# Optimization experiments

Measured on AMD Instinct MI355X. Metric: run time of the kernel, lower is better.

## Reference

```python
import jax, jax.numpy as jnp
import numpy as np
from jax import lax

B, N, D_FEAT = 16, 4096, 20
NPOINT, NSAMPLE = 1024, 32
MLP = [64, 64, 128]
IN_CH = 3 + 1 + D_FEAT  # grouped_xyz_norm(3) + L2 norm(1) + grouped_depth_norm(20)
BN_EPS = 1e-5


def setup_inputs() -> dict:
    key = jax.random.key(0)
    ks = jax.random.split(key, 20)
    inp = {
        "xyz": jax.random.normal(ks[0], (B, 3, N), dtype=jnp.float32),
        "feature": jax.random.normal(ks[1], (B, N, D_FEAT), dtype=jnp.float32),
    }
    last = IN_CH
    kidx = 2
    for li, out_ch in enumerate(MLP):
        inp[f"w{li}"] = jax.random.normal(ks[kidx], (out_ch, last), dtype=jnp.float32) * (1.0 / np.sqrt(last)); kidx += 1
        inp[f"b{li}"] = jax.random.normal(ks[kidx], (out_ch,), dtype=jnp.float32) * 0.01; kidx += 1
        inp[f"g{li}"] = 1.0 + 0.1 * jax.random.normal(ks[kidx], (out_ch,), dtype=jnp.float32); kidx += 1
        inp[f"bt{li}"] = 0.1 * jax.random.normal(ks[kidx], (out_ch,), dtype=jnp.float32); kidx += 1
        last = out_ch
    return inp


def square_distance(src, dst):
    # [B,S,C] x [B,M,C] -> [B,S,M]
    d = -2.0 * jnp.einsum("bsc,bmc->bsm", src, dst)
    d = d + jnp.sum(src * src, -1)[:, :, None]
    d = d + jnp.sum(dst * dst, -1)[:, None, :]
    return d


def farthest_point_sample(pts, npoint):
    # pts: [B,N,C]; deterministic start at index 0 (torch uses random start)
    b, n, _ = pts.shape
    bidx = jnp.arange(b)

    def step(carry, _):
        dist, far = carry
        centroid = pts[bidx, far]                      # [B,C]
        d = jnp.sum((pts - centroid[:, None, :]) ** 2, -1)  # [B,N]
        dist = jnp.minimum(dist, d)
        nxt = jnp.argmax(dist, -1)
        return (dist, nxt), far

    init = (jnp.full((b, n), 1e10, pts.dtype), jnp.zeros((b,), jnp.int32))
    _, idx = lax.scan(step, init, None, length=npoint)
    return idx.T  # [B,npoint]


def _gather_groups(points, idx):
    # points [B,N,C], idx [B,S,K] -> [B,S,K,C]
    return jax.vmap(lambda p, i: p[i])(points, idx)


def conv_bn_relu(x, w, b, g, bt):
    # x [B,C,K,S]; 1x1 conv = channel matmul; BN in training mode (batch stats, biased var)
    y = jnp.einsum("bcks,oc->boks", x, w) + b[None, :, None, None]
    mu = jnp.mean(y, axis=(0, 2, 3), keepdims=True)
    var = jnp.mean((y - mu) ** 2, axis=(0, 2, 3), keepdims=True)
    y = (y - mu) * lax.rsqrt(var + BN_EPS)
    y = y * g[None, :, None, None] + bt[None, :, None, None]
    return jax.nn.relu(y)


def reference(xyz, feature, w0, b0, g0, bt0, w1, b1, g1, bt1, w2, b2, g2, bt2):
    xyz_n = jnp.transpose(xyz, (0, 2, 1))              # [B,N,3]
    combined = jnp.concatenate([xyz_n, feature], -1)   # [B,N,23]
    fps_idx = farthest_point_sample(combined, NPOINT)  # [B,S]

    new_bin = jnp.take_along_axis(feature, fps_idx[:, :, None], axis=1)  # [B,S,20]
    new_xyz = jnp.take_along_axis(xyz_n, fps_idx[:, :, None], axis=1)    # [B,S,3]

    sqd = square_distance(new_bin, feature) + square_distance(new_xyz, xyz_n)  # [B,S,N]
    idx = jnp.argsort(sqd, axis=-1)[:, :, :NSAMPLE]    # [B,S,K]

    gxyz = _gather_groups(xyz_n, idx)                  # [B,S,K,3]
    gfeat = _gather_groups(feature, idx)               # [B,S,K,20]
    gxyz_norm = gxyz - new_xyz[:, :, None, :]
    gdep_norm = gfeat - new_bin[:, :, None, :]
    nrm = jnp.sqrt(jnp.maximum(jnp.sum(gxyz_norm ** 2, -1, keepdims=True), 1e-12))
    new_points = jnp.concatenate([gxyz_norm, nrm, gdep_norm], -1)  # [B,S,K,24]

    x = jnp.transpose(new_points, (0, 3, 2, 1))        # [B,24,K,S]
    for (w, b, g, bt) in [(w0, b0, g0, bt0), (w1, b1, g1, bt1), (w2, b2, g2, bt2)]:
        x = conv_bn_relu(x, w, b, g, bt)
    out = jnp.max(x, axis=2)                           # [B,128,S]
    return jnp.transpose(new_xyz, (0, 2, 1)), out, new_bin
```

## Files before the change

kernel.cpp:

```cpp
#include <hip/hip_runtime.h>

#define BB 16
#define NN 4096
#define DFEAT 20
#define SS 1024
#define KK 32
#define MM (BB*SS*KK)

#define WS_STATS   0ull
#define WS_PARAMS  8192ull
#define WS_FPSIDX  12288ull
#define WS_CENT    81920ull
#define WS_KNN     1654784ull
#define WS_COMB    3751936ull
#define WS_YB      10043392ull
#define WS_NEED    77152256ull

typedef float v2f __attribute__((ext_vector_type(2)));

static __device__ __forceinline__ unsigned short f2bf(float f){
    unsigned u = __float_as_uint(f);
    unsigned r = (u + 0x7FFFu + ((u >> 16) & 1u)) >> 16;
    return (unsigned short)r;
}
static __device__ __forceinline__ float bf2f(unsigned short v){
    return __uint_as_float((unsigned)v << 16);
}
static __device__ __forceinline__ void pinv2(v2f& x){
    asm volatile("" : "+v"(x));
}

template<int CTRL>
static __device__ __forceinline__ unsigned dpp32_or0(unsigned x){
    return (unsigned)__builtin_amdgcn_update_dpp(0, (int)x, CTRL, 0xf, 0xf, true);
}
static __device__ __forceinline__ unsigned umax32(unsigned a, unsigned b){
    return a > b ? a : b;
}
static __device__ __forceinline__ unsigned wave_max_u32(unsigned x){
    x = umax32(x, dpp32_or0<0x111>(x));
    x = umax32(x, dpp32_or0<0x112>(x));
    x = umax32(x, dpp32_or0<0x114>(x));
    x = umax32(x, dpp32_or0<0x118>(x));
    x = umax32(x, dpp32_or0<0x142>(x));
    x = umax32(x, dpp32_or0<0x143>(x));
    return x;
}

__global__ void k_zstats(double* __restrict__ stats){
    int t = threadIdx.x;
#pragma unroll
    for (int i = 0; i < 4; ++i) stats[i*256 + t] = 0.0;
}

__global__ void k_fail(float* __restrict__ out, int n){
    int i = blockIdx.x * 256 + threadIdx.x;
    if (i < n) out[i] = 0.f;
}

__global__ __launch_bounds__(256) void k_build(const float* __restrict__ xyz,
                                               const float* __restrict__ feat,
                                               float* __restrict__ comb)
{
    int idx = blockIdx.x * 256 + threadIdx.x;
    int b = idx >> 12, j = idx & 4095;
    float c[24];
    c[0] = xyz[((size_t)b*3 + 0)*NN + j];
    c[1] = xyz[((size_t)b*3 + 1)*NN + j];
    c[2] = xyz[((size_t)b*3 + 2)*NN + j];
    const float* f = feat + ((size_t)b*NN + j)*DFEAT;
#pragma unroll
    for (int d = 0; d < 20; ++d) c[3+d] = f[d];
    c[23] = 0.f;
    float* out = comb + (size_t)idx * 24;
#pragma unroll
    for (int q = 0; q < 6; ++q)
        ((float4*)out)[q] = make_float4(c[4*q], c[4*q+1], c[4*q+2], c[4*q+3]);
}

__global__ __launch_bounds__(512, 2) void k_fps(const float* __restrict__ comb,
                                                int* __restrict__ fpsidx)
{
    int b = blockIdx.x, t = threadIdx.x;
    const float* C = comb + (size_t)b * NN * 24;
    v2f pt2[4][24];
    v2f dist2[4];
#pragma unroll
    for (int p = 0; p < 8; ++p){
        const float4* r = (const float4*)(C + (size_t)(t + 512*p) * 24);
#pragma unroll
        for (int q = 0; q < 6; ++q){
            float4 v = r[q];
            pt2[p>>1][4*q+0][p&1] = v.x;
            pt2[p>>1][4*q+1][p&1] = v.y;
            pt2[p>>1][4*q+2][p&1] = v.z;
            pt2[p>>1][4*q+3][p&1] = v.w;
        }
    }
#pragma unroll
    for (int k = 0; k < 4; ++k){
        dist2[k] = (v2f){1e10f, 1e10f};
#pragma unroll
        for (int q = 0; q < 23; ++q) pinv2(pt2[k][q]);
    }

    __shared__ __align__(16) float wpt[2][8][24];
    __shared__ unsigned long long gkey[4];
    __shared__ int fps_lds[SS];
    int lane = t & 63, w = t >> 6;
    unsigned nt = 0xFFFFFFFFu - (unsigned)t;
    int far = 0;

    if (t < 4) gkey[t] = 0ull;

    float cc[24];
    {
        const float4* crow = (const float4*)C;
#pragma unroll
        for (int q = 0; q < 6; ++q){
            float4 cv = crow[q];
            cc[4*q] = cv.x; cc[4*q+1] = cv.y; cc[4*q+2] = cv.z; cc[4*q+3] = cv.w;
        }
    }
    __syncthreads();

    for (int s = 0; s < SS; ++s){
        if (t == 0) fps_lds[s] = far;
        v2f acc2[4];
#pragma unroll
        for (int k = 0; k < 4; ++k){
            v2f d0 = pt2[k][0] - cc[0];
            acc2[k] = d0 * d0;
        }
#pragma unroll
        for (int q = 1; q < 23; ++q){
            float cq = cc[q];
#pragma unroll
            for (int k = 0; k < 4; ++k){
                v2f dd = pt2[k][q] - cq;
                acc2[k] = __builtin_elementwise_fma(dd, dd, acc2[k]);
            }
        }
#pragma unroll
        for (int k = 0; k < 4; ++k)
            dist2[k] = __builtin_elementwise_min(dist2[k], acc2[k]);
        v2f m01 = __builtin_elementwise_max(dist2[0], dist2[1]);
        v2f m23 = __builtin_elementwise_max(dist2[2], dist2[3]);
        v2f mt  = __builtin_elementwise_max(m01, m23);
        float mf = fmaxf(mt[0], mt[1]);
        unsigned maxbits = __float_as_uint(mf);
        int pstar = 0;
#pragma unroll
        for (int p = 7; p >= 0; --p)
            if (__float_as_uint(dist2[p>>1][p&1]) == maxbits) pstar = p;

        unsigned M = __builtin_amdgcn_readlane((int)wave_max_u32(maxbits), 63);
        unsigned cidx = (maxbits == M) ? (nt - ((unsigned)pstar << 9)) : 0u;
        unsigned widxc = __builtin_amdgcn_readlane((int)wave_max_u32(cidx), 63);
        unsigned widx  = 0xFFFFFFFFu - widxc;

        int par = s & 1;
        if (t == (int)(widx & 511u)){
            int pw = (int)(widx >> 9);
            float* dst = wpt[par][w];
            switch (pw){
#define PE(P,q) pt2[(P)>>1][q][(P)&1]
#define STASH(P) case P: \
                ((float4*)dst)[0] = make_float4(PE(P,0),PE(P,1),PE(P,2),PE(P,3)); \
                ((float4*)dst)[1] = make_float4(PE(P,4),PE(P,5),PE(P,6),PE(P,7)); \
                ((float4*)dst)[2] = make_float4(PE(P,8),PE(P,9),PE(P,10),PE(P,11)); \
                ((float4*)dst)[3] = make_float4(PE(P,12),PE(P,13),PE(P,14),PE(P,15)); \
                ((float4*)dst)[4] = make_float4(PE(P,16),PE(P,17),PE(P,18),PE(P,19)); \
                ((float4*)dst)[5] = make_float4(PE(P,20),PE(P,21),PE(P,22),0.f); \
                break;
            STASH(0) STASH(1) STASH(2) STASH(3)
            STASH(4) STASH(5) STASH(6) STASH(7)
#undef STASH
#undef PE
            }
        }
        if (lane == 63){
            unsigned long long key = ((unsigned long long)M << 32)
                                   | (unsigned long long)widxc;
            atomicMax(&gkey[s & 3], key);
        }
        __syncthreads();
        unsigned long long k2 = gkey[s & 3];
        if (t == 0) gkey[(s + 2) & 3] = 0ull;
        far = (int)(0xFFFFFFFFu - (unsigned)(k2 & 0xFFFFFFFFull));
        int wg = (far & 511) >> 6;
        const float4* crow = (const float4*)wpt[par][wg];
#pragma unroll
        for (int q = 0; q < 6; ++q){
            float4 cv = crow[q];
            cc[4*q] = cv.x; cc[4*q+1] = cv.y; cc[4*q+2] = cv.z; cc[4*q+3] = cv.w;
        }
    }
    __syncthreads();
    fpsidx[b*SS + t]        = fps_lds[t];
    fpsidx[b*SS + 512 + t]  = fps_lds[512 + t];
}

__global__ __launch_bounds__(256) void k_gather(const float* __restrict__ comb,
                                                const int* __restrict__ fpsidx,
                                                float* __restrict__ cent,
                                                float* __restrict__ out0,
                                                float* __restrict__ out2)
{
    int idx = blockIdx.x * 256 + threadIdx.x;
    int b = idx >> 10, s = idx & 1023;
    int j = fpsidx[idx];
    const float* row = comb + ((size_t)b*NN + j) * 24;
    float* cr = cent + (size_t)idx * 24;
#pragma unroll
    for (int q = 0; q < 6; ++q) ((float4*)cr)[q] = ((const float4*)row)[q];
#pragma unroll
    for (int c = 0; c < 3; ++c) out0[((size_t)b*3 + c)*SS + s] = row[c];
    float* o2 = out2 + (size_t)idx * 20;
#pragma unroll
    for (int d = 0; d < 20; ++d) o2[d] = row[3 + d];
}

__global__ __launch_bounds__(256) void k_knn(const float* __restrict__ comb,
                                             const float* __restrict__ cent,
                                             int* __restrict__ knn)
{
    int w = threadIdx.x >> 6, lane = threadIdx.x & 63;
    int r = blockIdx.x * 4 + w;
    int b = r >> 10;
    const float* crow = cent + (size_t)r * 24;
    const float* P0 = comb + (size_t)b * NN * 24;
    double cc[24];
#pragma unroll
    for (int q = 0; q < 24; ++q) cc[q] = (double)crow[q];
    unsigned u[64];
#pragma unroll
    for (int k = 0; k < 64; ++k){
        int j = k*64 + lane;
        const float4* pr = (const float4*)(P0 + (size_t)j * 24);
        double acc = 0.0;
#pragma unroll
        for (int q = 0; q < 6; ++q){
            float4 v = pr[q];
            double d0 = (double)v.x - cc[4*q];
            double d1 = (double)v.y - cc[4*q+1];
            double d2 = (double)v.z - cc[4*q+2];
            double d3 = (double)v.w - cc[4*q+3];
            acc += d0*d0; acc += d1*d1; acc += d2*d2; acc += d3*d3;
        }
        u[k] = __float_as_uint((float)acc);
    }
    unsigned lo = 0u, hi = 0xFFFFFFFFu;
    for (int it = 0; it < 32; ++it){
        unsigned mid = lo + ((hi - lo) >> 1);
        int cnt = 0;
#pragma unroll
        for (int k = 0; k < 64; ++k) cnt += (u[k] <= mid) ? 1 : 0;
#pragma unroll
        for (int off = 32; off > 0; off >>= 1) cnt += __shfl_xor(cnt, off);
        if (cnt >= KK) hi = mid; else lo = mid + 1;
    }
    unsigned T = lo;
    int* orow = knn + (size_t)r * KK;
    unsigned long long lmask = (1ull << lane) - 1ull;
    int pos = 0;
#pragma unroll
    for (int k = 0; k < 64; ++k){
        bool lt = (u[k] < T);
        unsigned long long mk = __ballot(lt);
        if (lt) orow[pos + __popcll(mk & lmask)] = k*64 + lane;
        pos += __popcll(mk);
    }
#pragma unroll
    for (int k = 0; k < 64; ++k){
        if (pos >= KK) break;
        bool eq = (u[k] == T);
        unsigned long long mk = __ballot(eq);
        int rk = __popcll(mk & lmask);
        if (eq && (pos + rk) < KK) orow[pos + rk] = k*64 + lane;
        pos += __popcll(mk);
    }
}

__global__ __launch_bounds__(256) void k_l1(const float* __restrict__ comb,
                                            const float* __restrict__ cent,
                                            const int* __restrict__ knn,
                                            const float* __restrict__ w0,
                                            const float* __restrict__ b0,
                                            unsigned short* __restrict__ yb)
{
    __shared__ float Wt[24][64];
    __shared__ float Xt[24][68];
    int t = threadIdx.x;
    int m_base = blockIdx.x * 64;
    for (int i = t; i < 1536; i += 256){
        int o = i / 24, c = i - o*24;
        Wt[c][o] = w0[i];
    }
    {
        int sm = t & 63, g = t >> 6;
        int m = m_base + sm;
        int b = m >> 15;
        int row = m >> 5;
        int j = knn[m];
        const float* P  = comb + ((size_t)b*NN + j) * 24;
        const float* Cc = cent + (size_t)row * 24;
        if (g == 0){
            float dx = P[0]-Cc[0], dy = P[1]-Cc[1], dz = P[2]-Cc[2];
            Xt[0][sm] = dx; Xt[1][sm] = dy; Xt[2][sm] = dz;
            float n2 = dx*dx; n2 = fmaf(dy, dy, n2); n2 = fmaf(dz, dz, n2);
            Xt[3][sm] = sqrtf(fmaxf(n2, 1e-12f));
            Xt[4][sm] = P[3] - Cc[3];
            Xt[5][sm] = P[4] - Cc[4];
        } else {
#pragma unroll
            for (int cq = 0; cq < 6; ++cq){
                int c = 6*g + cq;
                Xt[c][sm] = P[c-1] - Cc[c-1];
            }
        }
    }
    __syncthreads();
    int i = t >> 4, jj = t & 15;
    float acc[4][4] = {};
#pragma unroll
    for (int c = 0; c < 24; ++c){
        float4 wv = *(const float4*)&Wt[c][i*4];
        float4 xv = *(const float4*)&Xt[c][jj*4];
        float wr[4] = {wv.x, wv.y, wv.z, wv.w};
        float xr[4] = {xv.x, xv.y, xv.z, xv.w};
#pragma unroll
        for (int a = 0; a < 4; ++a)
#pragma unroll
            for (int q = 0; q < 4; ++q) acc[a][q] = fmaf(wr[a], xr[q], acc[a][q]);
    }
#pragma unroll
    for (int oi = 0; oi < 4; ++oi){
        int o = i*4 + oi;
        float bb = b0[o];
        ushort4 rv;
        rv.x = f2bf(acc[oi][0]+bb); rv.y = f2bf(acc[oi][1]+bb);
        rv.z = f2bf(acc[oi][2]+bb); rv.w = f2bf(acc[oi][3]+bb);
        *(ushort4*)&yb[(size_t)o*MM + m_base + jj*4] = rv;
    }
}

__global__ __launch_bounds__(256) void k_stats(const unsigned short* __restrict__ y,
                                               double* __restrict__ stats)
{
    const int chunks = 8;
    int c = blockIdx.x / chunks, ch = blockIdx.x % chunks;
    size_t base = (size_t)c * MM + (size_t)ch * (MM / chunks);
    double s1 = 0.0, s2 = 0.0;
    const unsigned short* p = y + base;
    for (int i = threadIdx.x; i < MM/chunks; i += 256){
        float v = bf2f(p[i]);
        s1 += v; s2 += (double)v * v;
    }
#pragma unroll
    for (int off = 32; off > 0; off >>= 1){
        s1 += __shfl_xor(s1, off);
        s2 += __shfl_xor(s2, off);
    }
    __shared__ double ps1[4], ps2[4];
    int w = threadIdx.x >> 6, lane = threadIdx.x & 63;
    if (lane == 0){ ps1[w] = s1; ps2[w] = s2; }
    __syncthreads();
    if (threadIdx.x == 0){
        atomicAdd(&stats[c*2 + 0], ps1[0]+ps1[1]+ps1[2]+ps1[3]);
        atomicAdd(&stats[c*2 + 1], ps2[0]+ps2[1]+ps2[2]+ps2[3]);
    }
}

__global__ void k_affine(const double* __restrict__ stats, float* __restrict__ params, int C)
{
    int c = threadIdx.x;
    if (c < C){
        double mu = stats[c*2] / (double)MM;
        double var = stats[c*2 + 1] / (double)MM - mu*mu;
        params[c*2 + 0] = (float)mu;
        params[c*2 + 1] = (float)(1.0 / sqrt(var + 1e-5));
    }
}

__global__ __launch_bounds__(256) void k_l2(unsigned short* __restrict__ yb,
                                            const float* __restrict__ prm,
                                            const float* __restrict__ gg,
                                            const float* __restrict__ bt,
                                            const float* __restrict__ w,
                                            const float* __restrict__ bias)
{
    __shared__ float Wt[64][64];
    __shared__ float Xt[64][68];
    int t = threadIdx.x;
    int m_base = blockIdx.x * 64;
    for (int i = t; i < 4096; i += 256){
        int o = i >> 6, c = i & 63;
        Wt[c][o] = w[i];
    }
#pragma unroll
    for (int rp = 0; rp < 16; ++rp){
        int idx = rp*256 + t;
        int c = idx >> 6, mm2 = idx & 63;
        float v = bf2f(yb[(size_t)c*MM + m_base + mm2]);
        float t1 = (v - prm[c*2]) * prm[c*2 + 1];
        Xt[c][mm2] = fmaxf(fmaf(t1, gg[c], bt[c]), 0.f);
    }
    __syncthreads();
    int i = t >> 4, jj = t & 15;
    float acc[4][4] = {};
#pragma unroll
    for (int c = 0; c < 64; ++c){
        float4 wv = *(const float4*)&Wt[c][i*4];
        float4 xv = *(const float4*)&Xt[c][jj*4];
        float wr[4] = {wv.x, wv.y, wv.z, wv.w};
        float xr[4] = {xv.x, xv.y, xv.z, xv.w};
#pragma unroll
        for (int a = 0; a < 4; ++a)
#pragma unroll
            for (int q = 0; q < 4; ++q) acc[a][q] = fmaf(wr[a], xr[q], acc[a][q]);
    }
#pragma unroll
    for (int oi = 0; oi < 4; ++oi){
        int o = i*4 + oi;
        float bb = bias[o];
        ushort4 rv;
        rv.x = f2bf(acc[oi][0]+bb); rv.y = f2bf(acc[oi][1]+bb);
        rv.z = f2bf(acc[oi][2]+bb); rv.w = f2bf(acc[oi][3]+bb);
        *(ushort4*)&yb[(size_t)o*MM + m_base + jj*4] = rv;
    }
}

__global__ __launch_bounds__(256) void k_l3s(const unsigned short* __restrict__ yb,
                                             const float* __restrict__ prm,
                                             const float* __restrict__ gg,
                                             const float* __restrict__ bt,
                                             const float* __restrict__ w,
                                             const float* __restrict__ bias,
                                             double* __restrict__ stats)
{
    __shared__ float Wt[64][128];
    __shared__ float Xt[64][68];
    int t = threadIdx.x;
    for (int i = t; i < 8192; i += 256){
        int o = i >> 6, c = i & 63;
        Wt[c][o] = w[i];
    }
    int i = t >> 4, jj = t & 15;
    double s1[8] = {}, s2[8] = {};
    for (int tt = 0; tt < 16; ++tt){
        int m_base = (blockIdx.x * 16 + tt) * 64;
        __syncthreads();
#pragma unroll
        for (int rp = 0; rp < 16; ++rp){
            int idx = rp*256 + t;
            int c = idx >> 6, mm2 = idx & 63;
            float v = bf2f(yb[(size_t)c*MM + m_base + mm2]);
            float t1 = (v - prm[c*2]) * prm[c*2 + 1];
            Xt[c][mm2] = fmaxf(fmaf(t1, gg[c], bt[c]), 0.f);
        }
        __syncthreads();
        float acc[8][4] = {};
#pragma unroll
        for (int c = 0; c < 64; ++c){
            float4 w0v = *(const float4*)&Wt[c][i*8];
            float4 w1v = *(const float4*)&Wt[c][i*8 + 4];
            float4 xv  = *(const float4*)&Xt[c][jj*4];
            float wr[8] = {w0v.x, w0v.y, w0v.z, w0v.w, w1v.x, w1v.y, w1v.z, w1v.w};
            float xr[4] = {xv.x, xv.y, xv.z, xv.w};
#pragma unroll
            for (int a = 0; a < 8; ++a)
#pragma unroll
                for (int q = 0; q < 4; ++q) acc[a][q] = fmaf(wr[a], xr[q], acc[a][q]);
        }
#pragma unroll
        for (int oi = 0; oi < 8; ++oi){
            float bb = bias[i*8 + oi];
#pragma unroll
            for (int q = 0; q < 4; ++q){
                float v = acc[oi][q] + bb;
                s1[oi] += v;
                s2[oi] += (double)v * v;
            }
        }
    }
#pragma unroll
    for (int oi = 0; oi < 8; ++oi){
#pragma unroll
        for (int off = 1; off < 16; off <<= 1){
            s1[oi] += __shfl_xor(s1[oi], off);
            s2[oi] += __shfl_xor(s2[oi], off);
        }
    }
    if (jj == 0){
#pragma unroll
        for (int oi = 0; oi < 8; ++oi){
            int o = i*8 + oi;
            atomicAdd(&stats[o*2 + 0], s1[oi]);
            atomicAdd(&stats[o*2 + 1], s2[oi]);
        }
    }
}

__global__ __launch_bounds__(256) void k_final(const unsigned short* __restrict__ yb,
                                               const float* __restrict__ prm2,
                                               const float* __restrict__ g1c,
                                               const float* __restrict__ bt1c,
                                               const float* __restrict__ w,
                                               const float* __restrict__ bias,
                                               const float* __restrict__ prm3,
                                               const float* __restrict__ g2c,
                                               const float* __restrict__ bt2c,
                                               float* __restrict__ out1)
{
    __shared__ float Wt[64][128];
    __shared__ float Xt[64][68];
    int t = threadIdx.x;
    int m_base = blockIdx.x * 64;
    for (int i = t; i < 8192; i += 256){
        int o = i >> 6, c = i & 63;
        Wt[c][o] = w[i];
    }
#pragma unroll
    for (int rp = 0; rp < 16; ++rp){
        int idx = rp*256 + t;
        int c = idx >> 6, mm2 = idx & 63;
        float v = bf2f(yb[(size_t)c*MM + m_base + mm2]);
        float t1 = (v - prm2[c*2]) * prm2[c*2 + 1];
        Xt[c][mm2] = fmaxf(fmaf(t1, g1c[c], bt1c[c]), 0.f);
    }
    __syncthreads();
    int i = t >> 4, jj = t & 15;
    float acc[8][4] = {};
#pragma unroll
    for (int c = 0; c < 64; ++c){
        float4 w0v = *(const float4*)&Wt[c][i*8];
        float4 w1v = *(const float4*)&Wt[c][i*8 + 4];
        float4 xv  = *(const float4*)&Xt[c][jj*4];
        float wr[8] = {w0v.x, w0v.y, w0v.z, w0v.w, w1v.x, w1v.y, w1v.z, w1v.w};
        float xr[4] = {xv.x, xv.y, xv.z, xv.w};
#pragma unroll
        for (int a = 0; a < 8; ++a)
#pragma unroll
            for (int q = 0; q < 4; ++q) acc[a][q] = fmaf(wr[a], xr[q], acc[a][q]);
    }
    float mx[8];
#pragma unroll
    for (int oi = 0; oi < 8; ++oi){
        int o = i*8 + oi;
        float bb = bias[o];
        float mu = prm3[o*2], inv = prm3[o*2 + 1], gv = g2c[o], bv = bt2c[o];
        float m = 0.f;
#pragma unroll
        for (int q = 0; q < 4; ++q){
            float v = acc[oi][q] + bb;
            float r = fmaxf(fmaf((v - mu) * inv, gv, bv), 0.f);
            m = fmaxf(m, r);
        }
        mx[oi] = m;
    }
#pragma unroll
    for (int oi = 0; oi < 8; ++oi){
#pragma unroll
        for (int off = 1; off < 8; off <<= 1)
            mx[oi] = fmaxf(mx[oi], __shfl_xor(mx[oi], off));
    }
    if ((jj & 7) == 0){
        int rg = (m_base >> 5) + (jj >> 3);
        int b = rg >> 10, s = rg & 1023;
#pragma unroll
        for (int oi = 0; oi < 8; ++oi)
            out1[(size_t)b*131072 + (size_t)(i*8 + oi)*1024 + s] = mx[oi];
    }
}

extern "C" void kernel_launch(void* const* d_in, const int* in_sizes, int n_in,
                              void* d_out, int out_size, void* d_ws, size_t ws_size,
                              hipStream_t stream)
{
    const float* xyz  = (const float*)d_in[0];
    const float* feat = (const float*)d_in[1];
    const float* w0 = (const float*)d_in[2];  const float* b0  = (const float*)d_in[3];
    const float* g0 = (const float*)d_in[4];  const float* bt0 = (const float*)d_in[5];
    const float* w1 = (const float*)d_in[6];  const float* b1  = (const float*)d_in[7];
    const float* g1 = (const float*)d_in[8];  const float* bt1 = (const float*)d_in[9];
    const float* w2 = (const float*)d_in[10]; const float* b2  = (const float*)d_in[11];
    const float* g2 = (const float*)d_in[12]; const float* bt2 = (const float*)d_in[13];

    float* out0 = (float*)d_out;
    float* out1 = (float*)d_out + 49152;
    float* out2 = (float*)d_out + 49152 + 2097152;

    if (ws_size < WS_NEED){
        k_fail<<<(out_size + 255)/256, 256, 0, stream>>>((float*)d_out, out_size);
        return;
    }

    char* ws = (char*)d_ws;
    double* stats = (double*)(ws + WS_STATS);
    float* params = (float*)(ws + WS_PARAMS);
    int*   fpsidx = (int*)(ws + WS_FPSIDX);
    float* cent   = (float*)(ws + WS_CENT);
    int*   knn    = (int*)(ws + WS_KNN);
    float* comb   = (float*)(ws + WS_COMB);
    unsigned short* yb = (unsigned short*)(ws + WS_YB);

    k_zstats<<<1,    256, 0, stream>>>(stats);
    k_build <<<256,  256, 0, stream>>>(xyz, feat, comb);
    k_fps   <<<16,   512, 0, stream>>>(comb, fpsidx);
    k_gather<<<64,   256, 0, stream>>>(comb, fpsidx, cent, out0, out2);
    k_knn   <<<4096, 256, 0, stream>>>(comb, cent, knn);
    k_l1    <<<8192, 256, 0, stream>>>(comb, cent, knn, w0, b0, yb);
    k_stats <<<512,  256, 0, stream>>>(yb, stats);
    k_affine<<<1,    128, 0, stream>>>(stats, params, 64);
    k_l2    <<<8192, 256, 0, stream>>>(yb, params, g0, bt0, w1, b1);
    k_stats <<<512,  256, 0, stream>>>(yb, stats + 256);
    k_affine<<<1,    128, 0, stream>>>(stats + 256, params + 256, 64);
    k_l3s   <<<512,  256, 0, stream>>>(yb, params + 256, g1, bt1, w2, b2, stats + 512);
    k_affine<<<1,    128, 0, stream>>>(stats + 512, params + 512, 128);
    k_final <<<8192, 256, 0, stream>>>(yb, params + 256, g1, bt1, w2, b2,
                                       params + 512, g2, bt2, out1);
}
```

Baseline: 3.312 ms.

## Halve FPS block to 256 threads and replace LDS atomic argmax with per-wave keys

The farthest-point-sampling kernel now runs 256 threads per batch, each holding 16 points in registers instead of 8, so the block has 4 waves rather than 8. The cross-wave argmax no longer uses an LDS atomicMax on a rotating key slot. Each wave writes its key to a double-buffered slot, and every thread reduces the four keys after the barrier. This cuts barrier and atomic cost per serial iteration, but doubles per-thread ALU work and register pressure (about 400 VGPRs for points), which risks spills.

```diff
diff --git a/kernel.cpp b/kernel.cpp
--- a/kernel.cpp
+++ b/kernel.cpp
@@ -30,6 +30,9 @@
     asm volatile("" : "+v"(x));
 }
 
+static __device__ __forceinline__ unsigned long long max64(unsigned long long a, unsigned long long b){
+    return a > b ? a : b;
+}
 template<int CTRL>
 static __device__ __forceinline__ unsigned dpp32_or0(unsigned x){
     return (unsigned)__builtin_amdgcn_update_dpp(0, (int)x, CTRL, 0xf, 0xf, true);
@@ -78,16 +81,16 @@
         ((float4*)out)[q] = make_float4(c[4*q], c[4*q+1], c[4*q+2], c[4*q+3]);
 }
 
-__global__ __launch_bounds__(512, 2) void k_fps(const float* __restrict__ comb,
+__global__ __launch_bounds__(256, 1) void k_fps(const float* __restrict__ comb,
                                                 int* __restrict__ fpsidx)
 {
     int b = blockIdx.x, t = threadIdx.x;
     const float* C = comb + (size_t)b * NN * 24;
-    v2f pt2[4][24];
-    v2f dist2[4];
-#pragma unroll
-    for (int p = 0; p < 8; ++p){
-        const float4* r = (const float4*)(C + (size_t)(t + 512*p) * 24);
+    v2f pt2[8][24];
+    v2f dist2[8];
+#pragma unroll
+    for (int p = 0; p < 16; ++p){
+        const float4* r = (const float4*)(C + (size_t)(t + 256*p) * 24);
 #pragma unroll
         for (int q = 0; q < 6; ++q){
             float4 v = r[q];
@@ -98,21 +101,19 @@
         }
     }
 #pragma unroll
-    for (int k = 0; k < 4; ++k){
+    for (int k = 0; k < 8; ++k){
         dist2[k] = (v2f){1e10f, 1e10f};
 #pragma unroll
         for (int q = 0; q < 23; ++q) pinv2(pt2[k][q]);
     }
 
-    __shared__ __align__(16) float wpt[2][8][24];
-    __shared__ unsigned long long gkey[4];
+    __shared__ __align__(16) unsigned long long wkey[2][4];
+    __shared__ __align__(16) float wpt[2][4][24];
     __shared__ int fps_lds[SS];
     int lane = t & 63, w = t >> 6;
     unsigned nt = 0xFFFFFFFFu - (unsigned)t;
     int far = 0;
 
-    if (t < 4) gkey[t] = 0ull;
-
     float cc[24];
     {
         const float4* crow = (const float4*)C;
@@ -122,13 +123,12 @@
             cc[4*q] = cv.x; cc[4*q+1] = cv.y; cc[4*q+2] = cv.z; cc[4*q+3] = cv.w;
         }
     }
-    __syncthreads();
 
     for (int s = 0; s < SS; ++s){
         if (t == 0) fps_lds[s] = far;
-        v2f acc2[4];
-#pragma unroll
-        for (int k = 0; k < 4; ++k){
+        v2f acc2[8];
+#pragma unroll
+        for (int k = 0; k < 8; ++k){
             v2f d0 = pt2[k][0] - cc[0];
             acc2[k] = d0 * d0;
         }
@@ -136,32 +136,38 @@
         for (int q = 1; q < 23; ++q){
             float cq = cc[q];
 #pragma unroll
-            for (int k = 0; k < 4; ++k){
+            for (int k = 0; k < 8; ++k){
                 v2f dd = pt2[k][q] - cq;
                 acc2[k] = __builtin_elementwise_fma(dd, dd, acc2[k]);
             }
         }
 #pragma unroll
-        for (int k = 0; k < 4; ++k)
+        for (int k = 0; k < 8; ++k)
             dist2[k] = __builtin_elementwise_min(dist2[k], acc2[k]);
-        v2f m01 = __builtin_elementwise_max(dist2[0], dist2[1]);
-        v2f m23 = __builtin_elementwise_max(dist2[2], dist2[3]);
-        v2f mt  = __builtin_elementwise_max(m01, m23);
+        v2f m0 = __builtin_elementwise_max(dist2[0], dist2[1]);
+        v2f m1 = __builtin_elementwise_max(dist2[2], dist2[3]);
+        v2f m2 = __builtin_elementwise_max(dist2[4], dist2[5]);
+        v2f m3 = __builtin_elementwise_max(dist2[6], dist2[7]);
+        v2f n0 = __builtin_elementwise_max(m0, m1);
+        v2f n1 = __builtin_elementwise_max(m2, m3);
+        v2f mt = __builtin_elementwise_max(n0, n1);
         float mf = fmaxf(mt[0], mt[1]);
         unsigned maxbits = __float_as_uint(mf);
         int pstar = 0;
 #pragma unroll
-        for (int p = 7; p >= 0; --p)
+        for (int p = 15; p >= 0; --p)
             if (__float_as_uint(dist2[p>>1][p&1]) == maxbits) pstar = p;
 
         unsigned M = __builtin_amdgcn_readlane((int)wave_max_u32(maxbits), 63);
-        unsigned cidx = (maxbits == M) ? (nt - ((unsigned)pstar << 9)) : 0u;
+        unsigned cidx = (maxbits == M) ? (nt - ((unsigned)pstar << 8)) : 0u;
         unsigned widxc = __builtin_amdgcn_readlane((int)wave_max_u32(cidx), 63);
         unsigned widx  = 0xFFFFFFFFu - widxc;
 
         int par = s & 1;
-        if (t == (int)(widx & 511u)){
-            int pw = (int)(widx >> 9);
+        if (lane == 63)
+            wkey[par][w] = ((unsigned long long)M << 32) | (unsigned long long)widxc;
+        if (t == (int)(widx & 255u)){
+            int pw = (int)(widx >> 8);
             float* dst = wpt[par][w];
             switch (pw){
 #define PE(P,q) pt2[(P)>>1][q][(P)&1]
@@ -173,22 +179,20 @@
                 ((float4*)dst)[4] = make_float4(PE(P,16),PE(P,17),PE(P,18),PE(P,19)); \
                 ((float4*)dst)[5] = make_float4(PE(P,20),PE(P,21),PE(P,22),0.f); \
                 break;
-            STASH(0) STASH(1) STASH(2) STASH(3)
-            STASH(4) STASH(5) STASH(6) STASH(7)
+            STASH(0)  STASH(1)  STASH(2)  STASH(3)
+            STASH(4)  STASH(5)  STASH(6)  STASH(7)
+            STASH(8)  STASH(9)  STASH(10) STASH(11)
+            STASH(12) STASH(13) STASH(14) STASH(15)
 #undef STASH
 #undef PE
             }
         }
-        if (lane == 63){
-            unsigned long long key = ((unsigned long long)M << 32)
-                                   | (unsigned long long)widxc;
-            atomicMax(&gkey[s & 3], key);
-        }
         __syncthreads();
-        unsigned long long k2 = gkey[s & 3];
-        if (t == 0) gkey[(s + 2) & 3] = 0ull;
+        const ulonglong2* kp = (const ulonglong2*)wkey[par];
+        ulonglong2 q0 = kp[0], q1 = kp[1];
+        unsigned long long k2 = max64(max64(q0.x, q0.y), max64(q1.x, q1.y));
         far = (int)(0xFFFFFFFFu - (unsigned)(k2 & 0xFFFFFFFFull));
-        int wg = (far & 511) >> 6;
+        int wg = (far & 255) >> 6;
         const float4* crow = (const float4*)wpt[par][wg];
 #pragma unroll
         for (int q = 0; q < 6; ++q){
@@ -197,8 +201,9 @@
         }
     }
     __syncthreads();
-    fpsidx[b*SS + t]        = fps_lds[t];
-    fpsidx[b*SS + 512 + t]  = fps_lds[512 + t];
+#pragma unroll
+    for (int i = 0; i < 4; ++i)
+        fpsidx[b*SS + i*256 + t] = fps_lds[i*256 + t];
 }
 
 __global__ __launch_bounds__(256) void k_gather(const float* __restrict__ comb,
@@ -607,7 +612,7 @@
 
     k_zstats<<<1,    256, 0, stream>>>(stats);
     k_build <<<256,  256, 0, stream>>>(xyz, feat, comb);
-    k_fps   <<<16,   512, 0, stream>>>(comb, fpsidx);
+    k_fps   <<<16,   256, 0, stream>>>(comb, fpsidx);
     k_gather<<<64,   256, 0, stream>>>(comb, fpsidx, cent, out0, out2);
     k_knn   <<<4096, 256, 0, stream>>>(comb, cent, knn);
     k_l1    <<<8192, 256, 0, stream>>>(comb, cent, knn, w0, b0, yb);
```

Result: slower. 3.817 ms (+15.2%).
